# Kernel tuning notes

Measured on AMD Instinct MI355X. Metric: run time of the kernel, lower is better.

## Reference

```python
import jax, jax.numpy as jnp
import numpy as np

N_LINKS = 10000
N_PATHS = 50000
PLEN = 5                 # fixed path length -> max_len
E = N_PATHS * PLEN       # number of (link, path) edge entries
D = 32                   # link_state_dim == path_state_dim
H = 32
RU = 256                 # readout_units
T_ITERS = 8              # message-passing iterations t


def setup_inputs() -> dict:
    key = jax.random.key(0)
    ks = jax.random.split(key, 20)
    s = 0.1
    inp = {}
    inp["traffic"] = jax.random.uniform(ks[0], (N_PATHS,), dtype=jnp.float32)
    inp["packets"] = jax.random.uniform(ks[1], (N_PATHS,), dtype=jnp.float32)
    inp["time_dist_params"] = jax.random.normal(ks[2], (N_PATHS, 12), dtype=jnp.float32)
    inp["capacity"] = jax.random.uniform(ks[3], (N_LINKS,), dtype=jnp.float32)
    # edge lists: each path has exactly PLEN links
    inp["link_to_path"] = jax.random.randint(ks[4], (E,), 0, N_LINKS, dtype=jnp.int32)
    inp["path_ids"] = jnp.repeat(jnp.arange(N_PATHS, dtype=jnp.int32), PLEN)
    inp["sequence_path"] = jnp.tile(jnp.arange(PLEN, dtype=jnp.int32), N_PATHS)
    inp["path_to_link"] = jax.random.randint(ks[5], (E,), 0, N_PATHS, dtype=jnp.int32)
    inp["sequence_links"] = jax.random.randint(ks[6], (E,), 0, N_LINKS, dtype=jnp.int32)
    inp["n_links"] = N_LINKS
    inp["n_paths"] = N_PATHS
    # path-update GRU (input D -> hidden H), torch layout [3H, in]
    inp["Wi_p"] = jax.random.normal(ks[7], (3 * H, D), dtype=jnp.float32) * s
    inp["Wh_p"] = jax.random.normal(ks[8], (3 * H, H), dtype=jnp.float32) * s
    inp["bi_p"] = jnp.zeros((3 * H,), jnp.float32)
    inp["bh_p"] = jnp.zeros((3 * H,), jnp.float32)
    # link-update GRUCell (input H -> hidden D)
    inp["Wi_l"] = jax.random.normal(ks[9], (3 * D, H), dtype=jnp.float32) * s
    inp["Wh_l"] = jax.random.normal(ks[10], (3 * D, D), dtype=jnp.float32) * s
    inp["bi_l"] = jnp.zeros((3 * D,), jnp.float32)
    inp["bh_l"] = jnp.zeros((3 * D,), jnp.float32)
    # readout MLP
    inp["W1"] = jax.random.normal(ks[11], (RU, H), dtype=jnp.float32) * s
    inp["b1"] = jnp.zeros((RU,), jnp.float32)
    inp["W2"] = jax.random.normal(ks[12], (RU, RU), dtype=jnp.float32) * s
    inp["b2"] = jnp.zeros((RU,), jnp.float32)
    inp["W3"] = jax.random.normal(ks[13], (1, RU), dtype=jnp.float32) * s
    inp["b3"] = jnp.zeros((1,), jnp.float32)
    return inp


def _gru_step(x, h, Wi, Wh, bi, bh):
    # torch GRU gate math
    gi = x @ Wi.T + bi
    gh = h @ Wh.T + bh
    ir, iz, in_ = jnp.split(gi, 3, axis=-1)
    hr, hz, hn = jnp.split(gh, 3, axis=-1)
    r = jax.nn.sigmoid(ir + hr)
    z = jax.nn.sigmoid(iz + hz)
    n = jnp.tanh(in_ + r * hn)
    return (1.0 - z) * n + z * h


def reference(traffic, packets, time_dist_params, capacity,
              link_to_path, path_ids, sequence_path, path_to_link, sequence_links,
              n_links, n_paths,
              Wi_p, Wh_p, bi_p, bh_p, Wi_l, Wh_l, bi_l, bh_l,
              W1, b1, W2, b2, W3, b3):
    max_len = PLEN  # == sequence_path.max() + 1 (static)
    # per-path valid lengths (equivalent to the torch nonzero-row count loop)
    lens = jax.ops.segment_max(sequence_path, path_ids, num_segments=n_paths) + 1
    link_state = jnp.concatenate(
        [capacity[:, None], jnp.zeros((n_links, D - 1), capacity.dtype)], axis=1)
    path_state = jnp.concatenate(
        [traffic[:, None], packets[:, None], time_dist_params,
         jnp.zeros((n_paths, D - 14), traffic.dtype)], axis=1)

    for _ in range(T_ITERS):
        link_gather = link_state[link_to_path]  # [E, D]
        link_inputs = jnp.zeros((n_paths, max_len, D), link_state.dtype)
        link_inputs = link_inputs.at[path_ids, sequence_path].set(link_gather)

        def step(h, xt_t):
            xt, t = xt_t
            h_new = _gru_step(xt, h, Wi_p, Wh_p, bi_p, bh_p)
            h = jnp.where((t < lens)[:, None], h_new, h)  # pack_padded semantics
            return h, None

        path_state, _ = jax.lax.scan(
            step, path_state,
            (jnp.swapaxes(link_inputs, 0, 1), jnp.arange(max_len)))

        path_gather = path_state[path_to_link]  # [E, H]
        path_sum = jnp.zeros((n_links, H), path_gather.dtype).at[sequence_links].add(path_gather)
        link_state = _gru_step(path_sum, link_state, Wi_l, Wh_l, bi_l, bh_l)

    r = jax.nn.relu(path_state @ W1.T + b1)
    r = jax.nn.relu(r @ W2.T + b2)
    r = r @ W3.T + b3            # [n_paths, 1]
    return r[:, 0][None, :]      # [1, n_paths]
```

## Files before the change

### kernel.cpp

```cpp
#include <hip/hip_runtime.h>

#define NP 50000
#define NL 10000
#define PLEN 5
#define NE (NP * PLEN)
#define DD 32
#define RUU 256
#define TITERS 8
#define PPB 16
#define LPB 4
#define RPB 32

__device__ __forceinline__ float sigmoidf_(float a) {
    return 1.0f / (1.0f + __expf(-a));
}
__device__ __forceinline__ float tanhf_(float a) {
    a = fminf(fmaxf(a, -15.0f), 15.0f);
    float t = __expf(2.0f * a);
    return (t - 1.0f) / (t + 1.0f);
}

__global__ __launch_bounds__(256) void k_init(
    const float* __restrict__ traffic, const float* __restrict__ packets,
    const float* __restrict__ tdp, const float* __restrict__ capacity,
    float* __restrict__ path_state, float* __restrict__ link_state,
    int* __restrict__ lens, int* __restrict__ cnt) {
    int i = blockIdx.x * 256 + threadIdx.x;
    if (i < NP) {
        float v[DD];
        v[0] = traffic[i];
        v[1] = packets[i];
#pragma unroll
        for (int k = 0; k < 12; k++) v[2 + k] = tdp[i * 12 + k];
#pragma unroll
        for (int k = 14; k < DD; k++) v[k] = 0.0f;
#pragma unroll
        for (int k = 0; k < DD; k++) path_state[i * DD + k] = v[k];
        lens[i] = 0;
    }
    if (i < NL) {
        link_state[i * DD] = capacity[i];
#pragma unroll
        for (int k = 1; k < DD; k++) link_state[i * DD + k] = 0.0f;
        cnt[i] = 0;
    }
}

__global__ __launch_bounds__(256) void k_lens(const int* __restrict__ path_ids,
                                              const int* __restrict__ seq_path,
                                              int* __restrict__ lens) {
    int e = blockIdx.x * 256 + threadIdx.x;
    if (e < NE) atomicMax(&lens[path_ids[e]], seq_path[e] + 1);
}

__global__ __launch_bounds__(256) void k_csr_count(const int* __restrict__ seq_links,
                                                   int* __restrict__ cnt) {
    int e = blockIdx.x * 256 + threadIdx.x;
    if (e < NE) atomicAdd(&cnt[seq_links[e]], 1);
}

__global__ __launch_bounds__(256) void k_csr_scan(const int* __restrict__ cnt,
                                                  int* __restrict__ offs,
                                                  int* __restrict__ cursor) {
    __shared__ int ssum[256];
    const int tid = threadIdx.x;
    const int CH = 40;
    int base = tid * CH;
    int s = 0;
    for (int i = 0; i < CH; i++) {
        int idx = base + i;
        s += (idx < NL) ? cnt[idx] : 0;
    }
    ssum[tid] = s;
    __syncthreads();
    for (int off = 1; off < 256; off <<= 1) {
        int t = (tid >= off) ? ssum[tid - off] : 0;
        __syncthreads();
        ssum[tid] += t;
        __syncthreads();
    }
    int run = ssum[tid] - s;
    for (int i = 0; i < CH; i++) {
        int idx = base + i;
        if (idx < NL) {
            offs[idx] = run;
            cursor[idx] = run;
            run += cnt[idx];
        }
    }
    if (tid == 0) offs[NL] = ssum[255];
}

__global__ __launch_bounds__(256) void k_csr_fill(const int* __restrict__ seq_links,
                                                  const int* __restrict__ path_to_link,
                                                  int* __restrict__ cursor,
                                                  int* __restrict__ csr_pids) {
    int e = blockIdx.x * 256 + threadIdx.x;
    if (e < NE) {
        int l = seq_links[e];
        int slot = atomicAdd(&cursor[l], 1);
        csr_pids[slot] = path_to_link[e];
    }
}

__global__ __launch_bounds__(256) void k_w2t(const float* __restrict__ W2,
                                             float* __restrict__ W2t) {
    int j = blockIdx.x, k = threadIdx.x;
    W2t[k * RUU + j] = W2[j * RUU + k];
}

__global__ __launch_bounds__(256, 4) void k_gru_paths(
    const float* __restrict__ link_state, float* __restrict__ path_state,
    const int* __restrict__ link_to_path, const int* __restrict__ lens,
    const float* __restrict__ Wi, const float* __restrict__ Wh,
    const float* __restrict__ bi, const float* __restrict__ bh) {
    __shared__ float gi[PPB * PLEN * 96];
    __shared__ float hbuf[4][DD];
    const int tid = threadIdx.x;
    const int wave = tid >> 6;
    const int lane = tid & 63;
    const int d = lane & 31;
    const int half = lane >> 5;
    const int pl0 = wave * 4;
    const int pbase = blockIdx.x * PPB;

    float w[3][16];
#pragma unroll
    for (int g = 0; g < 3; g++) {
        const float* wp = &Wi[(g * 32 + d) * 32 + half * 16];
#pragma unroll
        for (int c = 0; c < 4; c++) *(float4*)&w[g][c * 4] = *(const float4*)&wp[c * 4];
    }
#pragma unroll
    for (int g = 0; g < 3; g++)
#pragma unroll
        for (int k = 0; k < 16; k++) asm volatile("" : "+v"(w[g][k]));
    {
        const float b0 = bi[d], b1_ = bi[d + 32], b2_ = bi[d + 64];
        int lia[4 * PLEN];
#pragma unroll
        for (int j = 0; j < 4; j++) {
            const int p = pbase + pl0 + j;
#pragma unroll
            for (int s = 0; s < PLEN; s++) lia[j * PLEN + s] = link_to_path[p * PLEN + s];
        }
        float xk[16];
#pragma unroll
        for (int c = 0; c < 4; c++)
            *(float4*)&xk[c * 4] =
                *(const float4*)&link_state[lia[0] * DD + half * 16 + c * 4];
#pragma unroll
        for (int u = 0; u < 20; u++) {
            float xn[16];
            if (u + 1 < 20) {
#pragma unroll
                for (int c = 0; c < 4; c++)
                    *(float4*)&xn[c * 4] =
                        *(const float4*)&link_state[lia[u + 1] * DD + half * 16 + c * 4];
            }
            float s0 = 0.f, s1 = 0.f, s2 = 0.f;
#pragma unroll
            for (int k = 0; k < 16; k++) {
                s0 = fmaf(xk[k], w[0][k], s0);
                s1 = fmaf(xk[k], w[1][k], s1);
                s2 = fmaf(xk[k], w[2][k], s2);
            }
            s0 += __shfl_xor(s0, 32);
            s1 += __shfl_xor(s1, 32);
            s2 += __shfl_xor(s2, 32);
            float* gp = &gi[(pl0 + (u / 5)) * (PLEN * 96) + (u % 5) * 96];
            gp[d]      = s0 + b0;
            gp[d + 32] = s1 + b1_;
            gp[d + 64] = s2 + b2_;
            if (u + 1 < 20) {
#pragma unroll
                for (int k = 0; k < 16; k++) xk[k] = xn[k];
            }
        }
    }
    __syncthreads();

#pragma unroll
    for (int g = 0; g < 3; g++) {
        const float* wp = &Wh[(g * 32 + d) * 32 + half * 16];
#pragma unroll
        for (int c = 0; c < 4; c++) *(float4*)&w[g][c * 4] = *(const float4*)&wp[c * 4];
    }
#pragma unroll
    for (int g = 0; g < 3; g++)
#pragma unroll
        for (int k = 0; k < 16; k++) asm volatile("" : "+v"(w[g][k]));
    const float bh0 = bh[d], bh1 = bh[d + 32], bh2 = bh[d + 64];

    for (int j = 0; j < 4; j++) {
        const int p = pbase + pl0 + j;
        const int len = lens[p];
        float hd = path_state[p * DD + d];
        float hk[16];
#pragma unroll
        for (int c = 0; c < 4; c++)
            *(float4*)&hk[c * 4] = *(const float4*)&path_state[p * DD + half * 16 + c * 4];
#pragma unroll
        for (int st = 0; st < PLEN; st++) {
            float hr = 0.f, hz = 0.f, hn = 0.f;
#pragma unroll
            for (int k = 0; k < 16; k++) {
                hr = fmaf(hk[k], w[0][k], hr);
                hz = fmaf(hk[k], w[1][k], hz);
                hn = fmaf(hk[k], w[2][k], hn);
            }
            hr += __shfl_xor(hr, 32);
            hz += __shfl_xor(hz, 32);
            hn += __shfl_xor(hn, 32);
            const float* gp = &gi[((pl0 + j) * PLEN + st) * 96];
            float gir = gp[d], giz = gp[d + 32], gin = gp[d + 64];
            float r = sigmoidf_(gir + hr + bh0);
            float z = sigmoidf_(giz + hz + bh1);
            float n = tanhf_(gin + r * (hn + bh2));
            float hnew = (1.0f - z) * n + z * hd;
            hd = (st < len) ? hnew : hd;
            hbuf[wave][d] = hd;
#pragma unroll
            for (int c = 0; c < 4; c++)
                *(float4*)&hk[c * 4] = *(const float4*)&hbuf[wave][half * 16 + c * 4];
        }
        if (half == 0) path_state[p * DD + d] = hd;
    }
}

__global__ __launch_bounds__(256, 4) void k_links(
    const float* __restrict__ path_state, float* __restrict__ link_state,
    const int* __restrict__ offs, const int* __restrict__ csr_pids,
    const float* __restrict__ Wi, const float* __restrict__ Wh,
    const float* __restrict__ bi, const float* __restrict__ bh) {
    __shared__ float xsum[4][DD];
    __shared__ float gil[4][96];
    const int tid = threadIdx.x;
    const int wave = tid >> 6;
    const int lane = tid & 63;
    const int d = lane & 31;
    const int half = lane >> 5;
    const int l = blockIdx.x * LPB + wave;

    float w[3][16];
#pragma unroll
    for (int g = 0; g < 3; g++) {
        const float* wp = &Wi[(g * 32 + d) * 32 + half * 16];
#pragma unroll
        for (int c = 0; c < 4; c++) *(float4*)&w[g][c * 4] = *(const float4*)&wp[c * 4];
    }
#pragma unroll
    for (int g = 0; g < 3; g++)
#pragma unroll
        for (int k = 0; k < 16; k++) asm volatile("" : "+v"(w[g][k]));

    const int beg = offs[l], end = offs[l + 1];
    float a0 = 0.f, a1 = 0.f, a2 = 0.f, a3 = 0.f;
    int t = beg + half;
    for (; t + 6 < end; t += 8) {
        int q0 = csr_pids[t];
        int q1 = csr_pids[t + 2];
        int q2 = csr_pids[t + 4];
        int q3 = csr_pids[t + 6];
        a0 += path_state[q0 * DD + d];
        a1 += path_state[q1 * DD + d];
        a2 += path_state[q2 * DD + d];
        a3 += path_state[q3 * DD + d];
    }
    for (; t < end; t += 2) a0 += path_state[csr_pids[t] * DD + d];
    float xv = (a0 + a1) + (a2 + a3);
    xv += __shfl_xor(xv, 32);
    xsum[wave][d] = xv;
    __syncthreads();

    {
        const float b0 = bi[d], b1_ = bi[d + 32], b2_ = bi[d + 64];
        float xk[16];
#pragma unroll
        for (int c = 0; c < 4; c++)
            *(float4*)&xk[c * 4] = *(const float4*)&xsum[wave][half * 16 + c * 4];
        float s0 = 0.f, s1 = 0.f, s2 = 0.f;
#pragma unroll
        for (int k = 0; k < 16; k++) {
            s0 = fmaf(xk[k], w[0][k], s0);
            s1 = fmaf(xk[k], w[1][k], s1);
            s2 = fmaf(xk[k], w[2][k], s2);
        }
        s0 += __shfl_xor(s0, 32);
        s1 += __shfl_xor(s1, 32);
        s2 += __shfl_xor(s2, 32);
        gil[wave][d]      = s0 + b0;
        gil[wave][d + 32] = s1 + b1_;
        gil[wave][d + 64] = s2 + b2_;
    }
    __syncthreads();

#pragma unroll
    for (int g = 0; g < 3; g++) {
        const float* wp = &Wh[(g * 32 + d) * 32 + half * 16];
#pragma unroll
        for (int c = 0; c < 4; c++) *(float4*)&w[g][c * 4] = *(const float4*)&wp[c * 4];
    }
#pragma unroll
    for (int g = 0; g < 3; g++)
#pragma unroll
        for (int k = 0; k < 16; k++) asm volatile("" : "+v"(w[g][k]));
    const float bh0 = bh[d], bh1 = bh[d + 32], bh2 = bh[d + 64];
    {
        float hd = link_state[l * DD + d];
        float hk[16];
#pragma unroll
        for (int c = 0; c < 4; c++)
            *(float4*)&hk[c * 4] = *(const float4*)&link_state[l * DD + half * 16 + c * 4];
        float hr = 0.f, hz = 0.f, hn = 0.f;
#pragma unroll
        for (int k = 0; k < 16; k++) {
            hr = fmaf(hk[k], w[0][k], hr);
            hz = fmaf(hk[k], w[1][k], hz);
            hn = fmaf(hk[k], w[2][k], hn);
        }
        hr += __shfl_xor(hr, 32);
        hz += __shfl_xor(hz, 32);
        hn += __shfl_xor(hn, 32);
        float gir = gil[wave][d], giz = gil[wave][d + 32], gin = gil[wave][d + 64];
        float r = sigmoidf_(gir + hr + bh0);
        float z = sigmoidf_(giz + hz + bh1);
        float n = tanhf_(gin + r * (hn + bh2));
        float hnew = (1.0f - z) * n + z * hd;
        if (half == 0) link_state[l * DD + d] = hnew;
    }
}

__global__ __launch_bounds__(256, 4) void k_readout(
    const float* __restrict__ path_state, float* __restrict__ out,
    const float* __restrict__ W1, const float* __restrict__ b1,
    const float* __restrict__ W2t, const float* __restrict__ b2,
    const float* __restrict__ W3, const float* __restrict__ b3) {
    __shared__ float sr1[RPB * RUU];
    const int tid = threadIdx.x;
    const int p0 = blockIdx.x * RPB;

    float w1r[DD];
#pragma unroll
    for (int c = 0; c < 8; c++)
        *(float4*)&w1r[c * 4] = *(const float4*)&W1[tid * DD + c * 4];
    float bb1 = b1[tid];

#pragma unroll 2
    for (int m = 0; m < RPB; m++) {
        int p = p0 + m;
        if (p >= NP) p = NP - 1;
        const float4* xr = (const float4*)&path_state[(size_t)p * DD];
        float acc = bb1;
#pragma unroll
        for (int c = 0; c < 8; c++) {
            float4 xv = xr[c];
            acc = fmaf(xv.x, w1r[c * 4 + 0], fmaf(xv.y, w1r[c * 4 + 1],
                  fmaf(xv.z, w1r[c * 4 + 2], fmaf(xv.w, w1r[c * 4 + 3], acc))));
        }
        sr1[m * RUU + tid] = fmaxf(acc, 0.0f);
    }
    __syncthreads();

    const int pig = tid >> 5;
    const int jg  = tid & 31;
    float accs[4][8];
#pragma unroll
    for (int jj = 0; jj < 8; jj++) {
        float bv = b2[jg * 8 + jj];
#pragma unroll
        for (int pp = 0; pp < 4; pp++) accs[pp][jj] = bv;
    }
    for (int k4 = 0; k4 < 64; k4++) {
        const int k0 = k4 * 4;
        float a[4][4];
#pragma unroll
        for (int pp = 0; pp < 4; pp++)
            *(float4*)&a[pp][0] = *(const float4*)&sr1[(pig * 4 + pp) * RUU + k0];
#pragma unroll
        for (int kk = 0; kk < 4; kk++) {
            float4 w0 = *(const float4*)&W2t[(size_t)(k0 + kk) * RUU + jg * 8];
            float4 w1_ = *(const float4*)&W2t[(size_t)(k0 + kk) * RUU + jg * 8 + 4];
#pragma unroll
            for (int pp = 0; pp < 4; pp++) {
                float av = a[pp][kk];
                accs[pp][0] = fmaf(av, w0.x, accs[pp][0]);
                accs[pp][1] = fmaf(av, w0.y, accs[pp][1]);
                accs[pp][2] = fmaf(av, w0.z, accs[pp][2]);
                accs[pp][3] = fmaf(av, w0.w, accs[pp][3]);
                accs[pp][4] = fmaf(av, w1_.x, accs[pp][4]);
                accs[pp][5] = fmaf(av, w1_.y, accs[pp][5]);
                accs[pp][6] = fmaf(av, w1_.z, accs[pp][6]);
                accs[pp][7] = fmaf(av, w1_.w, accs[pp][7]);
            }
        }
    }

    float w3r[8];
#pragma unroll
    for (int c = 0; c < 2; c++)
        *(float4*)&w3r[c * 4] = *(const float4*)&W3[jg * 8 + c * 4];
    float val[4];
#pragma unroll
    for (int pp = 0; pp < 4; pp++) {
        float v = 0.f;
#pragma unroll
        for (int jj = 0; jj < 8; jj++) v = fmaf(w3r[jj], fmaxf(accs[pp][jj], 0.f), v);
        val[pp] = v;
    }
#pragma unroll
    for (int m = 1; m < 32; m <<= 1)
#pragma unroll
        for (int pp = 0; pp < 4; pp++) val[pp] += __shfl_xor(val[pp], m);
    if (jg == 0) {
        float b3v = b3[0];
#pragma unroll
        for (int pp = 0; pp < 4; pp++) {
            int p = p0 + pig * 4 + pp;
            if (p < NP) out[p] = val[pp] + b3v;
        }
    }
}

extern "C" void kernel_launch(void* const* d_in, const int* in_sizes, int n_in,
                              void* d_out, int out_size, void* d_ws, size_t ws_size,
                              hipStream_t stream) {
    const float* traffic  = (const float*)d_in[0];
    const float* packets  = (const float*)d_in[1];
    const float* tdp      = (const float*)d_in[2];
    const float* capacity = (const float*)d_in[3];
    const int* link_to_path = (const int*)d_in[4];
    const int* path_ids     = (const int*)d_in[5];
    const int* seq_path     = (const int*)d_in[6];
    const int* path_to_link = (const int*)d_in[7];
    const int* seq_links    = (const int*)d_in[8];
    const float* Wi_p = (const float*)d_in[11];
    const float* Wh_p = (const float*)d_in[12];
    const float* bi_p = (const float*)d_in[13];
    const float* bh_p = (const float*)d_in[14];
    const float* Wi_l = (const float*)d_in[15];
    const float* Wh_l = (const float*)d_in[16];
    const float* bi_l = (const float*)d_in[17];
    const float* bh_l = (const float*)d_in[18];
    const float* W1 = (const float*)d_in[19];
    const float* b1 = (const float*)d_in[20];
    const float* W2 = (const float*)d_in[21];
    const float* b2 = (const float*)d_in[22];
    const float* W3 = (const float*)d_in[23];
    const float* b3 = (const float*)d_in[24];
    float* out = (float*)d_out;

    float* path_state = (float*)d_ws;
    float* link_state = path_state + (size_t)NP * DD;
    float* w2t        = link_state + (size_t)NL * DD;
    int* lens     = (int*)(w2t + RUU * RUU);
    int* cnt      = lens + NP;
    int* offs     = cnt + NL;
    int* cursor   = offs + NL + 1;
    int* csr_pids = cursor + NL;

    k_init<<<(NP + 255) / 256, 256, 0, stream>>>(traffic, packets, tdp, capacity,
                                                 path_state, link_state, lens, cnt);
    k_lens<<<(NE + 255) / 256, 256, 0, stream>>>(path_ids, seq_path, lens);
    k_csr_count<<<(NE + 255) / 256, 256, 0, stream>>>(seq_links, cnt);
    k_csr_scan<<<1, 256, 0, stream>>>(cnt, offs, cursor);
    k_csr_fill<<<(NE + 255) / 256, 256, 0, stream>>>(seq_links, path_to_link,
                                                     cursor, csr_pids);
    k_w2t<<<RUU, RUU, 0, stream>>>(W2, w2t);
    for (int t = 0; t < TITERS; t++) {
        k_gru_paths<<<NP / PPB, 256, 0, stream>>>(
            link_state, path_state, link_to_path, lens, Wi_p, Wh_p, bi_p, bh_p);
        k_links<<<NL / LPB, 256, 0, stream>>>(
            path_state, link_state, offs, csr_pids, Wi_l, Wh_l, bi_l, bh_l);
    }
    k_readout<<<(NP + RPB - 1) / RPB, 256, 0, stream>>>(path_state, out, W1, b1,
                                                        w2t, b2, W3, b3);
}
```

Measured before the change: 1.304 ms.

## Fuse message-passing iterations into one persistent cooperative kernel with grid syncs

Replaces the 16 separate path and link kernel launches with one cooperative persistent kernel of 512 blocks. Blocks loop over path and link chunks and use grid.sync between phases. This removes launch overhead and tail gaps between kernels, at the cost of reduced parallelism (512 blocks) and re-loading weights per chunk. It falls back to the old launches if the cooperative launch fails.

```diff
diff --git a/kernel.cpp b/kernel.cpp
--- a/kernel.cpp
+++ b/kernel.cpp
@@ -1,4 +1,7 @@
 #include <hip/hip_runtime.h>
+#include <hip/hip_cooperative_groups.h>
+
+namespace cg = cooperative_groups;
 
 #define NP 50000
 #define NL 10000
@@ -10,6 +13,7 @@
 #define PPB 16
 #define LPB 4
 #define RPB 32
+#define NBLK 512
 
 __device__ __forceinline__ float sigmoidf_(float a) {
     return 1.0f / (1.0f + __expf(-a));
@@ -109,21 +113,15 @@
     W2t[k * RUU + j] = W2[j * RUU + k];
 }
 
-__global__ __launch_bounds__(256, 4) void k_gru_paths(
+
+__device__ __forceinline__ void path_chunk_body(
+    int pbase, int pl0, int wave, int d, int half,
     const float* __restrict__ link_state, float* __restrict__ path_state,
     const int* __restrict__ link_to_path, const int* __restrict__ lens,
     const float* __restrict__ Wi, const float* __restrict__ Wh,
-    const float* __restrict__ bi, const float* __restrict__ bh) {
-    __shared__ float gi[PPB * PLEN * 96];
-    __shared__ float hbuf[4][DD];
-    const int tid = threadIdx.x;
-    const int wave = tid >> 6;
-    const int lane = tid & 63;
-    const int d = lane & 31;
-    const int half = lane >> 5;
-    const int pl0 = wave * 4;
-    const int pbase = blockIdx.x * PPB;
-
+    const float* __restrict__ bi, const float* __restrict__ bh,
+    float (*gi)[1], float (*hbuf)[DD]) {
+    float* gibase = (float*)gi;
     float w[3][16];
 #pragma unroll
     for (int g = 0; g < 3; g++) {
@@ -168,7 +166,7 @@
             s0 += __shfl_xor(s0, 32);
             s1 += __shfl_xor(s1, 32);
             s2 += __shfl_xor(s2, 32);
-            float* gp = &gi[(pl0 + (u / 5)) * (PLEN * 96) + (u % 5) * 96];
+            float* gp = &gibase[(pl0 + (u / 5)) * (PLEN * 96) + (u % 5) * 96];
             gp[d]      = s0 + b0;
             gp[d + 32] = s1 + b1_;
             gp[d + 64] = s2 + b2_;
@@ -212,7 +210,7 @@
             hr += __shfl_xor(hr, 32);
             hz += __shfl_xor(hz, 32);
             hn += __shfl_xor(hn, 32);
-            const float* gp = &gi[((pl0 + j) * PLEN + st) * 96];
+            const float* gp = &gibase[((pl0 + j) * PLEN + st) * 96];
             float gir = gp[d], giz = gp[d + 32], gin = gp[d + 64];
             float r = sigmoidf_(gir + hr + bh0);
             float z = sigmoidf_(giz + hz + bh1);
@@ -226,22 +224,16 @@
         }
         if (half == 0) path_state[p * DD + d] = hd;
     }
-}
-
-__global__ __launch_bounds__(256, 4) void k_links(
+    __syncthreads();
+}
+
+__device__ __forceinline__ void link_body(
+    int l, int wave, int d, int half,
     const float* __restrict__ path_state, float* __restrict__ link_state,
     const int* __restrict__ offs, const int* __restrict__ csr_pids,
     const float* __restrict__ Wi, const float* __restrict__ Wh,
-    const float* __restrict__ bi, const float* __restrict__ bh) {
-    __shared__ float xsum[4][DD];
-    __shared__ float gil[4][96];
-    const int tid = threadIdx.x;
-    const int wave = tid >> 6;
-    const int lane = tid & 63;
-    const int d = lane & 31;
-    const int half = lane >> 5;
-    const int l = blockIdx.x * LPB + wave;
-
+    const float* __restrict__ bi, const float* __restrict__ bh,
+    float (*xsum)[DD], float (*gil)[96]) {
     float w[3][16];
 #pragma unroll
     for (int g = 0; g < 3; g++) {
@@ -329,6 +321,68 @@
         float hnew = (1.0f - z) * n + z * hd;
         if (half == 0) link_state[l * DD + d] = hnew;
     }
+    __syncthreads();
+}
+
+__global__ __launch_bounds__(256, 4) void k_loop(
+    float* __restrict__ path_state, float* __restrict__ link_state,
+    const int* __restrict__ link_to_path, const int* __restrict__ lens,
+    const int* __restrict__ offs, const int* __restrict__ csr_pids,
+    const float* __restrict__ Wi_p, const float* __restrict__ Wh_p,
+    const float* __restrict__ bi_p, const float* __restrict__ bh_p,
+    const float* __restrict__ Wi_l, const float* __restrict__ Wh_l,
+    const float* __restrict__ bi_l, const float* __restrict__ bh_l) {
+    cg::grid_group grid = cg::this_grid();
+    __shared__ float gi[PPB * PLEN * 96];
+    __shared__ float hbuf[4][DD];
+    __shared__ float xsum[4][DD];
+    __shared__ float gil[4][96];
+    const int tid = threadIdx.x;
+    const int wave = tid >> 6;
+    const int lane = tid & 63;
+    const int d = lane & 31;
+    const int half = lane >> 5;
+    const int pl0 = wave * 4;
+    const int NCHUNK_P = NP / PPB;
+    const int NCHUNK_L = NL / 4;
+
+    for (int it = 0; it < TITERS; it++) {
+        for (int chunk = blockIdx.x; chunk < NCHUNK_P; chunk += NBLK)
+            path_chunk_body(chunk * PPB, pl0, wave, d, half, link_state,
+                            path_state, link_to_path, lens, Wi_p, Wh_p, bi_p,
+                            bh_p, (float(*)[1])gi, hbuf);
+        grid.sync();
+        for (int chunk = blockIdx.x; chunk < NCHUNK_L; chunk += NBLK)
+            link_body(chunk * 4 + wave, wave, d, half, path_state, link_state,
+                      offs, csr_pids, Wi_l, Wh_l, bi_l, bh_l, xsum, gil);
+        grid.sync();
+    }
+}
+
+__global__ __launch_bounds__(256, 4) void k_gru_paths(
+    const float* __restrict__ link_state, float* __restrict__ path_state,
+    const int* __restrict__ link_to_path, const int* __restrict__ lens,
+    const float* __restrict__ Wi, const float* __restrict__ Wh,
+    const float* __restrict__ bi, const float* __restrict__ bh) {
+    __shared__ float gi[PPB * PLEN * 96];
+    __shared__ float hbuf[4][DD];
+    const int tid = threadIdx.x;
+    path_chunk_body(blockIdx.x * PPB, (tid >> 6) * 4, tid >> 6, tid & 31,
+                    (tid & 63) >> 5, link_state, path_state, link_to_path, lens,
+                    Wi, Wh, bi, bh, (float(*)[1])gi, hbuf);
+}
+
+__global__ __launch_bounds__(256, 4) void k_links(
+    const float* __restrict__ path_state, float* __restrict__ link_state,
+    const int* __restrict__ offs, const int* __restrict__ csr_pids,
+    const float* __restrict__ Wi, const float* __restrict__ Wh,
+    const float* __restrict__ bi, const float* __restrict__ bh) {
+    __shared__ float xsum[4][DD];
+    __shared__ float gil[4][96];
+    const int tid = threadIdx.x;
+    link_body(blockIdx.x * LPB + (tid >> 6), tid >> 6, tid & 31,
+              (tid & 63) >> 5, path_state, link_state, offs, csr_pids, Wi, Wh,
+              bi, bh, xsum, gil);
 }
 
 __global__ __launch_bounds__(256, 4) void k_readout(
@@ -467,12 +521,28 @@
     k_csr_fill<<<(NE + 255) / 256, 256, 0, stream>>>(seq_links, path_to_link,
                                                      cursor, csr_pids);
     k_w2t<<<RUU, RUU, 0, stream>>>(W2, w2t);
-    for (int t = 0; t < TITERS; t++) {
-        k_gru_paths<<<NP / PPB, 256, 0, stream>>>(
-            link_state, path_state, link_to_path, lens, Wi_p, Wh_p, bi_p, bh_p);
-        k_links<<<NL / LPB, 256, 0, stream>>>(
-            path_state, link_state, offs, csr_pids, Wi_l, Wh_l, bi_l, bh_l);
-    }
+
+    {
+        void* args[] = {
+            (void*)&path_state, (void*)&link_state,
+            (void*)&link_to_path, (void*)&lens,
+            (void*)&offs, (void*)&csr_pids,
+            (void*)&Wi_p, (void*)&Wh_p, (void*)&bi_p, (void*)&bh_p,
+            (void*)&Wi_l, (void*)&Wh_l, (void*)&bi_l, (void*)&bh_l};
+        hipError_t err = hipLaunchCooperativeKernel((void*)k_loop, dim3(NBLK),
+                                                    dim3(256), args, 0, stream);
+        if (err != hipSuccess) {
+            for (int t = 0; t < TITERS; t++) {
+                k_gru_paths<<<NP / PPB, 256, 0, stream>>>(
+                    link_state, path_state, link_to_path, lens, Wi_p, Wh_p,
+                    bi_p, bh_p);
+                k_links<<<NL / LPB, 256, 0, stream>>>(
+                    path_state, link_state, offs, csr_pids, Wi_l, Wh_l, bi_l,
+                    bh_l);
+            }
+        }
+    }
+
     k_readout<<<(NP + RPB - 1) / RPB, 256, 0, stream>>>(path_state, out, W1, b1,
                                                         w2t, b2, W3, b3);
 }
```

New measurement: 2.585 ms. 98.2% more time.
